# Optimization experiments

Measured on AMD Instinct MI355X. Metric: run time of the kernel, lower is better.

The kernel has to match this reference:

```python
import jax, jax.numpy as jnp
import numpy as np

S = 28
L_COORD = 5.0
L_NOOBJ = 0.5


def _xyxy(boxes):
    # boxes [..., 4] as (cx, cy, w, h); cx,cy in grid units -> /S
    x = boxes[..., 0] / S
    y = boxes[..., 1] / S
    w = boxes[..., 2]
    h = boxes[..., 3]
    return jnp.stack([x - 0.5 * w, y - 0.5 * h, x + 0.5 * w, y + 0.5 * h], axis=-1)


def _iou_pairwise(b1, b2):
    # elementwise IoU of aligned boxes (equivalent to diag(compute_iou(...)))
    lt = jnp.maximum(b1[..., :2], b2[..., :2])
    rb = jnp.minimum(b1[..., 2:], b2[..., 2:])
    wh = jnp.maximum(rb - lt, 0.0)
    inter = wh[..., 0] * wh[..., 1]
    a1 = (b1[..., 2] - b1[..., 0]) * (b1[..., 3] - b1[..., 1])
    a2 = (b2[..., 2] - b2[..., 0]) * (b2[..., 3] - b2[..., 1])
    denom = a1 + a2 - inter
    return inter / jnp.where(denom > 0, denom, 1.0)


def setup_inputs() -> dict:
    key = jax.random.key(0)
    k1, k2, k3, k4 = jax.random.split(key, 4)
    N = 1024
    pred_tensor = jax.random.uniform(k1, (N, S, S, 30), dtype=jnp.float32)
    target_boxes = jax.random.uniform(k2, (N, S, S, 4), dtype=jnp.float32)
    target_cls = jax.random.uniform(k3, (N, S, S, 20), dtype=jnp.float32)
    has_object_map = jax.random.bernoulli(k4, 0.3, (N, S, S))
    return {"pred_tensor": pred_tensor, "target_boxes": target_boxes,
            "target_cls": target_cls, "has_object_map": has_object_map}


def reference(pred_tensor, target_boxes, target_cls, has_object_map):
    N = pred_tensor.shape[0]
    mask = has_object_map            # (N,S,S) bool
    fm = mask.astype(pred_tensor.dtype)
    pb1 = pred_tensor[..., :5]
    pb2 = pred_tensor[..., 5:10]
    pred_cls = pred_tensor[..., 10:]

    # class loss: masked sum of squared errors over object cells
    cls_loss = jnp.sum(fm[..., None] * (pred_cls - target_cls) ** 2)

    # no-object loss: confidence of both boxes on non-object cells vs 0
    nfm = 1.0 - fm
    no_obj_loss = L_NOOBJ * jnp.sum(nfm * (pb1[..., 4] ** 2 + pb2[..., 4] ** 2))

    # per-cell IoU of each predicted box vs the target box
    tgt_xyxy = _xyxy(target_boxes)
    iou1 = _iou_pairwise(_xyxy(pb1[..., :4]), tgt_xyxy)
    iou2 = _iou_pairwise(_xyxy(pb2[..., :4]), tgt_xyxy)
    take1 = iou1 > iou2
    best_iou = jnp.where(take1, iou1, iou2)           # (N,S,S)
    best_box = jnp.where(take1[..., None], pb1, pb2)  # (N,S,S,5)

    xy_loss = jnp.sum(fm[..., None] * (best_box[..., :2] - target_boxes[..., :2]) ** 2)
    wh_p = jnp.sqrt(jnp.where(mask[..., None], best_box[..., 2:4], 1.0))
    wh_t = jnp.sqrt(jnp.where(mask[..., None], target_boxes[..., 2:4], 1.0))
    wh_loss = jnp.sum(fm[..., None] * (wh_p - wh_t) ** 2)
    reg_loss = L_COORD * (xy_loss + wh_loss)

    # containing-object confidence loss; target IoU is detached
    contain_obj_loss = jnp.sum(fm * (best_box[..., 4] - jax.lax.stop_gradient(best_iou)) ** 2)

    total_loss = cls_loss + no_obj_loss + contain_obj_loss + reg_loss
    return jnp.stack([total_loss, reg_loss, contain_obj_loss, no_obj_loss, cls_loss]) / N
```

## Files before the change

kernel.cpp:

```cpp
#include <hip/hip_runtime.h>


#define SS 28
#define BLOCK 256
#define CPB 256
#define PRED_F4_PER_BLOCK (CPB * 30 / 4)

__global__ __launch_bounds__(BLOCK) void yolo_main(
    const float4* __restrict__ pred4,
    const float4* __restrict__ tbox4,
    const float4* __restrict__ tcls4,
    const int*    __restrict__ mask,
    float4* __restrict__ block_part,
    int cells)
{
    __shared__ float p_sh[CPB * 30];

    const int t = threadIdx.x;
    const int blk = blockIdx.x;

    {
        const float4* src = pred4 + (size_t)blk * PRED_F4_PER_BLOCK;
        float4* dst = (float4*)p_sh;
        #pragma unroll
        for (int i = 0; i < 8; ++i) {
            int k = i * BLOCK + t;
            if (k < PRED_F4_PER_BLOCK)
                dst[k] = src[k];
        }
    }
    __syncthreads();

    const int cell = blk * CPB + t;

    float acc_cls = 0.f, acc_noobj = 0.f, acc_reg = 0.f, acc_cont = 0.f;

    if (cell < cells) {
        bool m = mask[cell] != 0;
        float fm = m ? 1.f : 0.f;
        float4 tb = tbox4[cell];

        float pr[30];
        {
            const float2* p2 = (const float2*)(p_sh + t * 30);
            #pragma unroll
            for (int i = 0; i < 15; ++i) {
                float2 v = p2[i];
                pr[2 * i] = v.x; pr[2 * i + 1] = v.y;
            }
        }

        {
            const float4* t4 = tcls4 + (size_t)cell * 5;
            float cls = 0.f;
            #pragma unroll
            for (int i = 0; i < 5; ++i) {
                float4 v = t4[i];
                float d0 = pr[10 + 4 * i + 0] - v.x;
                float d1 = pr[10 + 4 * i + 1] - v.y;
                float d2 = pr[10 + 4 * i + 2] - v.z;
                float d3 = pr[10 + 4 * i + 3] - v.w;
                cls += d0 * d0 + d1 * d1 + d2 * d2 + d3 * d3;
            }
            acc_cls = fm * cls;
        }

        acc_noobj = (1.f - fm) * (pr[4] * pr[4] + pr[9] * pr[9]);

        const float invS = 1.f / 28.f;
        float txc = tb.x * invS, tyc = tb.y * invS;
        float t0 = txc - 0.5f * tb.z, t1 = tyc - 0.5f * tb.w;
        float t2 = txc + 0.5f * tb.z, t3 = tyc + 0.5f * tb.w;
        float ta = (t2 - t0) * (t3 - t1);

        float b1xc = pr[0] * invS, b1yc = pr[1] * invS;
        float a0 = b1xc - 0.5f * pr[2], a1 = b1yc - 0.5f * pr[3];
        float a2 = b1xc + 0.5f * pr[2], a3 = b1yc + 0.5f * pr[3];
        float wx = fmaxf(fminf(a2, t2) - fmaxf(a0, t0), 0.f);
        float wy = fmaxf(fminf(a3, t3) - fmaxf(a1, t1), 0.f);
        float inter = wx * wy;
        float area1 = (a2 - a0) * (a3 - a1);
        float den = area1 + ta - inter;
        float iou1 = inter / (den > 0.f ? den : 1.f);

        float b2xc = pr[5] * invS, b2yc = pr[6] * invS;
        float c0 = b2xc - 0.5f * pr[7], c1 = b2yc - 0.5f * pr[8];
        float c2 = b2xc + 0.5f * pr[7], c3 = b2yc + 0.5f * pr[8];
        wx = fmaxf(fminf(c2, t2) - fmaxf(c0, t0), 0.f);
        wy = fmaxf(fminf(c3, t3) - fmaxf(c1, t1), 0.f);
        inter = wx * wy;
        float area2 = (c2 - c0) * (c3 - c1);
        den = area2 + ta - inter;
        float iou2 = inter / (den > 0.f ? den : 1.f);

        bool take1 = iou1 > iou2;
        float best_iou = take1 ? iou1 : iou2;
        float bbx = take1 ? pr[0] : pr[5];
        float bby = take1 ? pr[1] : pr[6];
        float bbw = take1 ? pr[2] : pr[7];
        float bbh = take1 ? pr[3] : pr[8];
        float bbc = take1 ? pr[4] : pr[9];

        float dx = bbx - tb.x, dy = bby - tb.y;
        float xy = dx * dx + dy * dy;

        float wp = m ? bbw : 1.f, hp = m ? bbh : 1.f;
        float wt = m ? tb.z : 1.f, ht = m ? tb.w : 1.f;
        float dw = sqrtf(wp) - sqrtf(wt);
        float dh = sqrtf(hp) - sqrtf(ht);
        float wh = dw * dw + dh * dh;

        acc_reg = fm * (xy + wh);

        float dc = bbc - best_iou;
        acc_cont = fm * dc * dc;
    }

    float4 v = make_float4(acc_cls, acc_noobj, acc_reg, acc_cont);
    #pragma unroll
    for (int off = 32; off >= 1; off >>= 1) {
        v.x += __shfl_down(v.x, off, 64);
        v.y += __shfl_down(v.y, off, 64);
        v.z += __shfl_down(v.z, off, 64);
        v.w += __shfl_down(v.w, off, 64);
    }
    __shared__ float4 sred[BLOCK / 64];
    int lane = threadIdx.x & 63;
    int wave = threadIdx.x >> 6;
    if (lane == 0) sred[wave] = v;
    __syncthreads();
    if (threadIdx.x == 0) {
        float4 r = sred[0];
        #pragma unroll
        for (int w = 1; w < BLOCK / 64; ++w) {
            r.x += sred[w].x; r.y += sred[w].y; r.z += sred[w].z; r.w += sred[w].w;
        }
        block_part[blockIdx.x] = r;
    }
}

__global__ __launch_bounds__(BLOCK) void yolo_final(
    const float4* __restrict__ part, int nparts, float* __restrict__ out, float invN)
{
    float4 v = make_float4(0.f, 0.f, 0.f, 0.f);
    for (int i = threadIdx.x; i < nparts; i += BLOCK) {
        float4 p = part[i];
        v.x += p.x; v.y += p.y; v.z += p.z; v.w += p.w;
    }
    #pragma unroll
    for (int off = 32; off >= 1; off >>= 1) {
        v.x += __shfl_down(v.x, off, 64);
        v.y += __shfl_down(v.y, off, 64);
        v.z += __shfl_down(v.z, off, 64);
        v.w += __shfl_down(v.w, off, 64);
    }
    __shared__ float4 sred[BLOCK / 64];
    int lane = threadIdx.x & 63;
    int wave = threadIdx.x >> 6;
    if (lane == 0) sred[wave] = v;
    __syncthreads();
    if (threadIdx.x == 0) {
        float4 r = sred[0];
        #pragma unroll
        for (int w = 1; w < BLOCK / 64; ++w) {
            r.x += sred[w].x; r.y += sred[w].y; r.z += sred[w].z; r.w += sred[w].w;
        }
        float cls    = r.x;
        float no_obj = 0.5f * r.y;
        float reg    = 5.0f * r.z;
        float cont   = r.w;
        float total  = cls + no_obj + cont + reg;
        out[0] = total  * invN;
        out[1] = reg    * invN;
        out[2] = cont   * invN;
        out[3] = no_obj * invN;
        out[4] = cls    * invN;
    }
}

extern "C" void kernel_launch(void* const* d_in, const int* in_sizes, int n_in,
                              void* d_out, int out_size, void* d_ws, size_t ws_size,
                              hipStream_t stream) {
    const float* pred = (const float*)d_in[0];
    const float* tbox = (const float*)d_in[1];
    const float* tcls = (const float*)d_in[2];
    const int*   mask = (const int*)d_in[3];
    float* out = (float*)d_out;

    int cells = in_sizes[0] / 30;
    int n_img = cells / (SS * SS);
    int nblocks = (cells + CPB - 1) / CPB;

    float4* part = (float4*)d_ws;

    yolo_main<<<nblocks, BLOCK, 0, stream>>>(
        (const float4*)pred, (const float4*)tbox, (const float4*)tcls,
        mask, part, cells);
    yolo_final<<<1, BLOCK, 0, stream>>>(part, nblocks, out, 1.0f / (float)n_img);
}
```

Before: 206.9 us.

## Use persistent grid with per-wave double-buffered async global-to-LDS staging

Replaces the one-block-per-256-cells launch with a fixed grid of 512 blocks. Each wave processes 64-cell chunks in a grid-stride loop and prefetches the next chunk's prediction data straight into LDS with global_load_lds while it computes the current one. The goal is to overlap memory latency with compute and drop the block-wide barrier and register round trip of the old staging copy. This relies on hand-written vmcnt waits whose counts must match the issued loads. The other loads (target boxes, classes, mask) stay synchronous and also raise vmcnt, which could make the wait count wrong or too strict.

```diff
diff --git a/kernel.cpp b/kernel.cpp
--- a/kernel.cpp
+++ b/kernel.cpp
@@ -1,48 +1,140 @@
 #include <hip/hip_runtime.h>
+#include <stdint.h>
 
 
 #define SS 28
 #define BLOCK 256
-#define CPB 256
-#define PRED_F4_PER_BLOCK (CPB * 30 / 4)
-
-__global__ __launch_bounds__(BLOCK) void yolo_main(
-    const float4* __restrict__ pred4,
+#define WPB 4
+#define CPW 64
+#define CHUNK_FLOATS (CPW * 30)
+#define GRID 512
+
+typedef const __attribute__((address_space(1))) void* gvp;
+typedef __attribute__((address_space(3))) void* lvp;
+
+#define WAITVM(n) __builtin_amdgcn_s_waitcnt(0x0F70 | (n))
+
+__device__ __forceinline__ void stage_chunk(const float* __restrict__ pred,
+                                            long long chunk, float* ldsbuf, int lane)
+{
+    const float* src = pred + chunk * CHUNK_FLOATS;
+    #pragma unroll
+    for (int k = 0; k < 7; ++k) {
+        __builtin_amdgcn_global_load_lds((gvp)(src + k * 256 + lane * 4),
+                                         (lvp)(ldsbuf + k * 256), 16, 0, 0);
+    }
+    #pragma unroll
+    for (int j = 0; j < 2; ++j) {
+        __builtin_amdgcn_global_load_lds((gvp)(src + 1792 + j * 64 + lane),
+                                         (lvp)(ldsbuf + 1792 + j * 64), 4, 0, 0);
+    }
+}
+
+__device__ __forceinline__ void cell_loss(
+    const float* __restrict__ pr,
+    float4 tb, const float4* __restrict__ tc4, bool m,
+    float& acc_cls, float& acc_noobj, float& acc_reg, float& acc_cont)
+{
+    float fm = m ? 1.f : 0.f;
+
+    float cls = 0.f;
+    #pragma unroll
+    for (int i = 0; i < 5; ++i) {
+        float4 v = tc4[i];
+        float d0 = pr[10 + 4 * i + 0] - v.x;
+        float d1 = pr[10 + 4 * i + 1] - v.y;
+        float d2 = pr[10 + 4 * i + 2] - v.z;
+        float d3 = pr[10 + 4 * i + 3] - v.w;
+        cls += d0 * d0 + d1 * d1 + d2 * d2 + d3 * d3;
+    }
+    acc_cls += fm * cls;
+
+    acc_noobj += (1.f - fm) * (pr[4] * pr[4] + pr[9] * pr[9]);
+
+    const float invS = 1.f / 28.f;
+    float txc = tb.x * invS, tyc = tb.y * invS;
+    float t0 = txc - 0.5f * tb.z, t1 = tyc - 0.5f * tb.w;
+    float t2 = txc + 0.5f * tb.z, t3 = tyc + 0.5f * tb.w;
+    float ta = (t2 - t0) * (t3 - t1);
+
+    float b1xc = pr[0] * invS, b1yc = pr[1] * invS;
+    float a0 = b1xc - 0.5f * pr[2], a1 = b1yc - 0.5f * pr[3];
+    float a2 = b1xc + 0.5f * pr[2], a3 = b1yc + 0.5f * pr[3];
+    float wx = fmaxf(fminf(a2, t2) - fmaxf(a0, t0), 0.f);
+    float wy = fmaxf(fminf(a3, t3) - fmaxf(a1, t1), 0.f);
+    float inter = wx * wy;
+    float area1 = (a2 - a0) * (a3 - a1);
+    float den = area1 + ta - inter;
+    float iou1 = inter / (den > 0.f ? den : 1.f);
+
+    float b2xc = pr[5] * invS, b2yc = pr[6] * invS;
+    float c0 = b2xc - 0.5f * pr[7], c1 = b2yc - 0.5f * pr[8];
+    float c2 = b2xc + 0.5f * pr[7], c3 = b2yc + 0.5f * pr[8];
+    wx = fmaxf(fminf(c2, t2) - fmaxf(c0, t0), 0.f);
+    wy = fmaxf(fminf(c3, t3) - fmaxf(c1, t1), 0.f);
+    inter = wx * wy;
+    float area2 = (c2 - c0) * (c3 - c1);
+    den = area2 + ta - inter;
+    float iou2 = inter / (den > 0.f ? den : 1.f);
+
+    bool take1 = iou1 > iou2;
+    float best_iou = take1 ? iou1 : iou2;
+    float bbx = take1 ? pr[0] : pr[5];
+    float bby = take1 ? pr[1] : pr[6];
+    float bbw = take1 ? pr[2] : pr[7];
+    float bbh = take1 ? pr[3] : pr[8];
+    float bbc = take1 ? pr[4] : pr[9];
+
+    float dx = bbx - tb.x, dy = bby - tb.y;
+    float xy = dx * dx + dy * dy;
+
+    float wp = m ? bbw : 1.f, hp = m ? bbh : 1.f;
+    float wt = m ? tb.z : 1.f, ht = m ? tb.w : 1.f;
+    float dw = sqrtf(wp) - sqrtf(wt);
+    float dh = sqrtf(hp) - sqrtf(ht);
+    float wh = dw * dw + dh * dh;
+
+    acc_reg += fm * (xy + wh);
+
+    float dc = bbc - best_iou;
+    acc_cont += fm * dc * dc;
+}
+
+__global__ __launch_bounds__(BLOCK, 2) void yolo_main(
+    const float*  __restrict__ pred,
     const float4* __restrict__ tbox4,
     const float4* __restrict__ tcls4,
     const int*    __restrict__ mask,
     float4* __restrict__ block_part,
-    int cells)
-{
-    __shared__ float p_sh[CPB * 30];
-
-    const int t = threadIdx.x;
-    const int blk = blockIdx.x;
-
-    {
-        const float4* src = pred4 + (size_t)blk * PRED_F4_PER_BLOCK;
-        float4* dst = (float4*)p_sh;
-        #pragma unroll
-        for (int i = 0; i < 8; ++i) {
-            int k = i * BLOCK + t;
-            if (k < PRED_F4_PER_BLOCK)
-                dst[k] = src[k];
-        }
-    }
-    __syncthreads();
-
-    const int cell = blk * CPB + t;
+    int nchunks, int cells)
+{
+    __shared__ float stage[WPB][2][CHUNK_FLOATS];
+    __shared__ float4 sred[WPB];
+
+    const int t    = threadIdx.x;
+    const int lane = t & 63;
+    const int w    = t >> 6;
+    const int gw   = blockIdx.x * WPB + w;
+    const int nw   = GRID * WPB;
 
     float acc_cls = 0.f, acc_noobj = 0.f, acc_reg = 0.f, acc_cont = 0.f;
 
-    if (cell < cells) {
-        bool m = mask[cell] != 0;
-        float fm = m ? 1.f : 0.f;
-        float4 tb = tbox4[cell];
+    int c = gw;
+    int buf = 0;
+    if (c < nchunks) stage_chunk(pred, (long long)c, &stage[w][0][0], lane);
+
+    while (c < nchunks) {
+        int cn = c + nw;
+        if (cn < nchunks) {
+            stage_chunk(pred, (long long)cn, &stage[w][buf ^ 1][0], lane);
+            WAITVM(9);
+        } else {
+            WAITVM(0);
+        }
 
         float pr[30];
         {
-            const float2* p2 = (const float2*)(p_sh + t * 30);
+            const float2* p2 = (const float2*)&stage[w][buf][lane * 30];
             #pragma unroll
             for (int i = 0; i < 15; ++i) {
                 float2 v = p2[i];
@@ -50,73 +142,60 @@
             }
         }
 
-        {
-            const float4* t4 = tcls4 + (size_t)cell * 5;
-            float cls = 0.f;
-            #pragma unroll
-            for (int i = 0; i < 5; ++i) {
-                float4 v = t4[i];
-                float d0 = pr[10 + 4 * i + 0] - v.x;
-                float d1 = pr[10 + 4 * i + 1] - v.y;
-                float d2 = pr[10 + 4 * i + 2] - v.z;
-                float d3 = pr[10 + 4 * i + 3] - v.w;
-                cls += d0 * d0 + d1 * d1 + d2 * d2 + d3 * d3;
-            }
-            acc_cls = fm * cls;
-        }
-
-        acc_noobj = (1.f - fm) * (pr[4] * pr[4] + pr[9] * pr[9]);
-
-        const float invS = 1.f / 28.f;
-        float txc = tb.x * invS, tyc = tb.y * invS;
-        float t0 = txc - 0.5f * tb.z, t1 = tyc - 0.5f * tb.w;
-        float t2 = txc + 0.5f * tb.z, t3 = tyc + 0.5f * tb.w;
-        float ta = (t2 - t0) * (t3 - t1);
-
-        float b1xc = pr[0] * invS, b1yc = pr[1] * invS;
-        float a0 = b1xc - 0.5f * pr[2], a1 = b1yc - 0.5f * pr[3];
-        float a2 = b1xc + 0.5f * pr[2], a3 = b1yc + 0.5f * pr[3];
-        float wx = fmaxf(fminf(a2, t2) - fmaxf(a0, t0), 0.f);
-        float wy = fmaxf(fminf(a3, t3) - fmaxf(a1, t1), 0.f);
-        float inter = wx * wy;
-        float area1 = (a2 - a0) * (a3 - a1);
-        float den = area1 + ta - inter;
-        float iou1 = inter / (den > 0.f ? den : 1.f);
-
-        float b2xc = pr[5] * invS, b2yc = pr[6] * invS;
-        float c0 = b2xc - 0.5f * pr[7], c1 = b2yc - 0.5f * pr[8];
-        float c2 = b2xc + 0.5f * pr[7], c3 = b2yc + 0.5f * pr[8];
-        wx = fmaxf(fminf(c2, t2) - fmaxf(c0, t0), 0.f);
-        wy = fmaxf(fminf(c3, t3) - fmaxf(c1, t1), 0.f);
-        inter = wx * wy;
-        float area2 = (c2 - c0) * (c3 - c1);
-        den = area2 + ta - inter;
-        float iou2 = inter / (den > 0.f ? den : 1.f);
-
-        bool take1 = iou1 > iou2;
-        float best_iou = take1 ? iou1 : iou2;
-        float bbx = take1 ? pr[0] : pr[5];
-        float bby = take1 ? pr[1] : pr[6];
-        float bbw = take1 ? pr[2] : pr[7];
-        float bbh = take1 ? pr[3] : pr[8];
-        float bbc = take1 ? pr[4] : pr[9];
-
-        float dx = bbx - tb.x, dy = bby - tb.y;
-        float xy = dx * dx + dy * dy;
-
-        float wp = m ? bbw : 1.f, hp = m ? bbh : 1.f;
-        float wt = m ? tb.z : 1.f, ht = m ? tb.w : 1.f;
-        float dw = sqrtf(wp) - sqrtf(wt);
-        float dh = sqrtf(hp) - sqrtf(ht);
-        float wh = dw * dw + dh * dh;
-
-        acc_reg = fm * (xy + wh);
-
-        float dc = bbc - best_iou;
-        acc_cont = fm * dc * dc;
+        int cell = c * CPW + lane;
+        bool m = mask[cell] != 0;
+        float4 tb = tbox4[cell];
+        cell_loss(pr, tb, tcls4 + (size_t)cell * 5, m,
+                  acc_cls, acc_noobj, acc_reg, acc_cont);
+
+        buf ^= 1;
+        c = cn;
+    }
+
+    int tail_base = nchunks * CPW;
+    if (gw == 0 && tail_base + lane < cells) {
+        int cell = tail_base + lane;
+        float pr[30];
+        const float2* p2 = (const float2*)(pred + (size_t)cell * 30);
+        #pragma unroll
+        for (int i = 0; i < 15; ++i) {
+            float2 v = p2[i];
+            pr[2 * i] = v.x; pr[2 * i + 1] = v.y;
+        }
+        bool m = mask[cell] != 0;
+        float4 tb = tbox4[cell];
+        cell_loss(pr, tb, tcls4 + (size_t)cell * 5, m,
+                  acc_cls, acc_noobj, acc_reg, acc_cont);
     }
 
     float4 v = make_float4(acc_cls, acc_noobj, acc_reg, acc_cont);
+    #pragma unroll
+    for (int off = 32; off >= 1; off >>= 1) {
+        v.x += __shfl_down(v.x, off, 64);
+        v.y += __shfl_down(v.y, off, 64);
+        v.z += __shfl_down(v.z, off, 64);
+        v.w += __shfl_down(v.w, off, 64);
+    }
+    if (lane == 0) sred[w] = v;
+    __syncthreads();
+    if (t == 0) {
+        float4 r = sred[0];
+        #pragma unroll
+        for (int i = 1; i < WPB; ++i) {
+            r.x += sred[i].x; r.y += sred[i].y; r.z += sred[i].z; r.w += sred[i].w;
+        }
+        block_part[blockIdx.x] = r;
+    }
+}
+
+__global__ __launch_bounds__(BLOCK) void yolo_final(
+    const float4* __restrict__ part, int nparts, float* __restrict__ out, float invN)
+{
+    float4 v = make_float4(0.f, 0.f, 0.f, 0.f);
+    for (int i = threadIdx.x; i < nparts; i += BLOCK) {
+        float4 p = part[i];
+        v.x += p.x; v.y += p.y; v.z += p.z; v.w += p.w;
+    }
     #pragma unroll
     for (int off = 32; off >= 1; off >>= 1) {
         v.x += __shfl_down(v.x, off, 64);
@@ -135,36 +214,6 @@
         for (int w = 1; w < BLOCK / 64; ++w) {
             r.x += sred[w].x; r.y += sred[w].y; r.z += sred[w].z; r.w += sred[w].w;
         }
-        block_part[blockIdx.x] = r;
-    }
-}
-
-__global__ __launch_bounds__(BLOCK) void yolo_final(
-    const float4* __restrict__ part, int nparts, float* __restrict__ out, float invN)
-{
-    float4 v = make_float4(0.f, 0.f, 0.f, 0.f);
-    for (int i = threadIdx.x; i < nparts; i += BLOCK) {
-        float4 p = part[i];
-        v.x += p.x; v.y += p.y; v.z += p.z; v.w += p.w;
-    }
-    #pragma unroll
-    for (int off = 32; off >= 1; off >>= 1) {
-        v.x += __shfl_down(v.x, off, 64);
-        v.y += __shfl_down(v.y, off, 64);
-        v.z += __shfl_down(v.z, off, 64);
-        v.w += __shfl_down(v.w, off, 64);
-    }
-    __shared__ float4 sred[BLOCK / 64];
-    int lane = threadIdx.x & 63;
-    int wave = threadIdx.x >> 6;
-    if (lane == 0) sred[wave] = v;
-    __syncthreads();
-    if (threadIdx.x == 0) {
-        float4 r = sred[0];
-        #pragma unroll
-        for (int w = 1; w < BLOCK / 64; ++w) {
-            r.x += sred[w].x; r.y += sred[w].y; r.z += sred[w].z; r.w += sred[w].w;
-        }
         float cls    = r.x;
         float no_obj = 0.5f * r.y;
         float reg    = 5.0f * r.z;
@@ -187,14 +236,13 @@
     const int*   mask = (const int*)d_in[3];
     float* out = (float*)d_out;
 
-    int cells = in_sizes[0] / 30;
-    int n_img = cells / (SS * SS);
-    int nblocks = (cells + CPB - 1) / CPB;
+    int cells   = in_sizes[0] / 30;
+    int n_img   = cells / (SS * SS);
+    int nchunks = cells / CPW;
 
     float4* part = (float4*)d_ws;
 
-    yolo_main<<<nblocks, BLOCK, 0, stream>>>(
-        (const float4*)pred, (const float4*)tbox, (const float4*)tcls,
-        mask, part, cells);
-    yolo_final<<<1, BLOCK, 0, stream>>>(part, nblocks, out, 1.0f / (float)n_img);
-}
+    yolo_main<<<GRID, BLOCK, 0, stream>>>(
+        pred, (const float4*)tbox, (const float4*)tcls, mask, part, nchunks, cells);
+    yolo_final<<<1, BLOCK, 0, stream>>>(part, GRID, out, 1.0f / (float)n_img);
+}
```

New measurement: 202.3 us. 2.3% less time.
